# Kernel tuning notes

Measured on AMD Instinct MI355X. Metric: run time of the kernel, lower is better.

Reference implementation:

```python
import jax, jax.numpy as jnp
import numpy as np
from jax import lax

PROB_THRESHOLD = 0.9
IOU_THRESHOLD = 0.5
H, W = 80, 80


def setup_inputs() -> dict:
    key = jax.random.key(0)
    # [5, H, W]: channel 0 = probability, channels 1:5 = (x1, y1, w, h)
    x = jax.random.uniform(key, (5, H, W), dtype=jnp.float32)
    return {"x": x}


def _pairwise_iou(boxes):
    # boxes: [N, 4] in xyxy format (torchvision box_iou semantics, no +1)
    area = jnp.maximum(boxes[:, 2] - boxes[:, 0], 0.0) * jnp.maximum(boxes[:, 3] - boxes[:, 1], 0.0)
    lt = jnp.maximum(boxes[:, None, :2], boxes[None, :, :2])  # [N, N, 2]
    rb = jnp.minimum(boxes[:, None, 2:], boxes[None, :, 2:])  # [N, N, 2]
    wh = jnp.maximum(rb - lt, 0.0)
    inter = wh[..., 0] * wh[..., 1]                           # [N, N]
    union = area[:, None] + area[None, :] - inter
    return inter / jnp.maximum(union, 1e-9)


def reference(x):
    # Flatten grid: rows = [prob, x1, y1, w, h]
    flat = x.reshape(5, -1).T  # [N, 5]
    valid = flat[:, 0] > PROB_THRESHOLD

    # Faithful in-place transform from the torch code:
    #   bbx[:, 2] = bbx[:, 0] + bbx[:, 2];  bbx[:, 3] = bbx[:, 1] + bbx[:, 3]
    # (column 0 is the probability channel, exactly as the source does it)
    c2 = flat[:, 0] + flat[:, 2]
    c3 = flat[:, 1] + flat[:, 3]
    b5 = jnp.stack([flat[:, 0], flat[:, 1], c2, c3, flat[:, 4]], axis=1)  # [N, 5]

    # Sort by score descending; invalid rows pushed to the end with -inf
    scores = jnp.where(valid, b5[:, 0], -jnp.inf)
    order = jnp.argsort(-scores)
    b5_sorted = b5[order]          # [N, 5]
    valid_sorted = valid[order]    # [N]
    boxes = b5_sorted[:, 1:]       # [N, 4] -> nms(boxes=x[:,1:], scores=x[:,0])

    iou = _pairwise_iou(boxes)     # [N, N], dominant 164 MB intermediate
    N = boxes.shape[0]

    # Greedy NMS in score order: keep box i iff it is valid and no already-kept
    # higher-scoring box overlaps it with IoU > threshold.
    def body(i, keep):
        suppressed = jnp.any(keep & (iou[i] > IOU_THRESHOLD))
        return keep.at[i].set(valid_sorted[i] & ~suppressed)

    keep = lax.fori_loop(0, N, body, jnp.zeros((N,), dtype=bool))

    # Fixed-shape, jit-friendly equivalent of x[bbxis]: kept rows (score-sorted),
    # suppressed / below-threshold rows zeroed out.
    return jnp.where(keep[:, None], b5_sorted, 0.0)
```

## Files before the change

### kernel.cpp

```cpp
#include <hip/hip_runtime.h>


#define MAXM  256
#define CHUNK 200

__global__ __launch_bounds__(256) void k_rankpart(
    const float* __restrict__ X, int* __restrict__ part,
    int* __restrict__ counters, int n, int groups, int chunks) {
  int b = blockIdx.x;
  if (b >= groups * chunks) {
    if (threadIdx.x < 8) counters[threadIdx.x] = 0;
    return;
  }
  int g = b / chunks, c = b - g * chunks;
  int i = g * 256 + threadIdx.x;
  int c0 = c * CHUNK, cend = min(c0 + CHUNK, n);
  float si = (i < n) ? X[i] : -1.f;
  int gt = 0, eq = 0;
  const float4* X4 = (const float4*)(X + c0);
  int nq = (cend - c0) >> 2;
  for (int q = 0; q < nq; ++q) {
    float4 v = X4[q];
    gt += (v.x > si) + (v.y > si) + (v.z > si) + (v.w > si);
    eq += (v.x == si) + (v.y == si) + (v.z == si) + (v.w == si);
  }
  for (int j = c0 + (nq << 2); j < cend; ++j) {
    float sj = X[j];
    gt += (sj > si); eq += (sj == si);
  }
  if (i >= c0 && i < cend) eq -= 1;
  int partial = gt;
  if (__any(eq > 0)) {
    int eqlt = 0;
    for (int j = c0; j < cend; ++j)
      eqlt += (X[j] == si) && (j < i);
    partial = gt + eqlt;
  }
  if (i < n) part[c * n + i] = partial;
}

__global__ __launch_bounds__(256) void k_finish(
    const float* __restrict__ X, const int* __restrict__ part,
    float* __restrict__ out, float* __restrict__ list,
    int* __restrict__ counters, int n, int chunks, int nblocks) {
  __shared__ int sfix;
  const int t = threadIdx.x;
  int i = blockIdx.x * 256 + t;
  if (i < n) {
    float s = X[i];
    int r = 0;
    for (int c = 0; c < chunks; ++c) r += part[c * n + i];
    float* row = out + (size_t)r * 5;
    if (s > 0.9f) {
      float f1 = X[n + i], f2 = X[2 * n + i], f3 = X[3 * n + i], f4 = X[4 * n + i];
      float c2 = s + f2, c3 = f1 + f3;
      row[0] = s; row[1] = f1; row[2] = c2; row[3] = c3; row[4] = f4;
      float w = fmaxf(c3 - f1, 0.f);
      float h = fmaxf(f4 - c2, 0.f);
      float area = w * h;
      if (area > 0.f) {
        int p = atomicAdd(&counters[0], 1);
        if (p < MAXM) {
          float* e = list + (size_t)p * 6;
          e[0] = __int_as_float(r);
          e[1] = f1; e[2] = c2; e[3] = c3; e[4] = f4; e[5] = area;
        }
      }
    } else {
      row[0] = 0.f; row[1] = 0.f; row[2] = 0.f; row[3] = 0.f; row[4] = 0.f;
    }
  }
  __threadfence();
  __syncthreads();
  if (t == 0) {
    int old = atomicAdd(&counters[1], 1);
    sfix = (old == nblocks - 1);
  }
  __syncthreads();
  if (!sfix) return;
  __threadfence();

  __shared__ int   srank[MAXM];
  __shared__ float sbox[MAXM][4];
  __shared__ float sarea[MAXM];
  __shared__ int   skeep[MAXM];
  __shared__ int   sflag;
  int M = __hip_atomic_load(&counters[0], __ATOMIC_ACQUIRE, __HIP_MEMORY_SCOPE_AGENT);
  if (M > MAXM) M = MAXM;
  for (int e = t; e < M; e += 256) {
    float v0 = __hip_atomic_load(&list[e * 6 + 0], __ATOMIC_RELAXED, __HIP_MEMORY_SCOPE_AGENT);
    int r = __float_as_int(v0);
    int pos = 0;
    for (int m = 0; m < M; ++m) {
      float vm = __hip_atomic_load(&list[m * 6 + 0], __ATOMIC_RELAXED, __HIP_MEMORY_SCOPE_AGENT);
      pos += (__float_as_int(vm) < r);
    }
    srank[pos] = r;
    sbox[pos][0] = __hip_atomic_load(&list[e * 6 + 1], __ATOMIC_RELAXED, __HIP_MEMORY_SCOPE_AGENT);
    sbox[pos][1] = __hip_atomic_load(&list[e * 6 + 2], __ATOMIC_RELAXED, __HIP_MEMORY_SCOPE_AGENT);
    sbox[pos][2] = __hip_atomic_load(&list[e * 6 + 3], __ATOMIC_RELAXED, __HIP_MEMORY_SCOPE_AGENT);
    sbox[pos][3] = __hip_atomic_load(&list[e * 6 + 4], __ATOMIC_RELAXED, __HIP_MEMORY_SCOPE_AGENT);
    sarea[pos]   = __hip_atomic_load(&list[e * 6 + 5], __ATOMIC_RELAXED, __HIP_MEMORY_SCOPE_AGENT);
    skeep[pos] = 1;
  }
  __syncthreads();
  for (int s = 1; s < M; ++s) {
    if (t == 0) sflag = 0;
    __syncthreads();
    if (t < s && skeep[t]) {
      float ltx = fmaxf(sbox[t][0], sbox[s][0]);
      float lty = fmaxf(sbox[t][1], sbox[s][1]);
      float rbx = fminf(sbox[t][2], sbox[s][2]);
      float rby = fminf(sbox[t][3], sbox[s][3]);
      float w = fmaxf(rbx - ltx, 0.f);
      float h = fmaxf(rby - lty, 0.f);
      float inter = w * h;
      float uni = sarea[t] + sarea[s] - inter;
      if (inter / fmaxf(uni, 1e-9f) > 0.5f) sflag = 1;
    }
    __syncthreads();
    if (t == 0 && sflag) skeep[s] = 0;
    __syncthreads();
  }
  for (int e = t; e < M; e += 256) {
    if (!skeep[e]) {
      float* row = out + (size_t)srank[e] * 5;
      row[0] = 0.f; row[1] = 0.f; row[2] = 0.f; row[3] = 0.f; row[4] = 0.f;
    }
  }
}

#define FB_NTH  1024
#define FB_MAXV 2048
__global__ __launch_bounds__(FB_NTH, 1) void nms_fallback(
    const float* __restrict__ X, float* __restrict__ out, int n, int out_n) {
  __shared__ float cscore[FB_MAXV];
  __shared__ unsigned int cidx[FB_MAXV];
  __shared__ int s_vcount, s_mcount, sflag;
  __shared__ int srank[MAXM];
  __shared__ float sbox[MAXM][4];
  __shared__ float sarea[MAXM];
  __shared__ int skeep[MAXM];
  __shared__ int prank[MAXM];
  __shared__ float pbox[MAXM][4];
  __shared__ float parea[MAXM];
  const int t = threadIdx.x;
  if (t == 0) { s_vcount = 0; s_mcount = 0; }
  float4* out4 = (float4*)out;
  int n4 = out_n >> 2;
  for (int i = t; i < n4; i += FB_NTH) out4[i] = make_float4(0.f, 0.f, 0.f, 0.f);
  for (int i = (n4 << 2) + t; i < out_n; i += FB_NTH) out[i] = 0.f;
  __syncthreads();
  for (int i = t; i < n; i += FB_NTH) {
    float s = X[i];
    if (s > 0.9f) {
      int p = atomicAdd(&s_vcount, 1);
      if (p < FB_MAXV) { cscore[p] = s; cidx[p] = (unsigned int)i; }
    }
  }
  __syncthreads();
  const int V = min(s_vcount, FB_MAXV);
  for (int e = t; e < V; e += FB_NTH) {
    float s = cscore[e];
    unsigned int idx = cidx[e];
    int rank = 0;
    for (int m = 0; m < V; ++m) {
      float sm = cscore[m];
      rank += (sm > s) || (sm == s && cidx[m] < idx);
    }
    float f1 = X[n + idx], f2 = X[2 * n + idx], f3 = X[3 * n + idx], f4 = X[4 * n + idx];
    float c2 = s + f2, c3 = f1 + f3;
    float* row = out + (size_t)rank * 5;
    row[0] = s; row[1] = f1; row[2] = c2; row[3] = c3; row[4] = f4;
    float w = fmaxf(c3 - f1, 0.f), h = fmaxf(f4 - c2, 0.f);
    float area = w * h;
    if (area > 0.f) {
      int p = atomicAdd(&s_mcount, 1);
      if (p < MAXM) {
        prank[p] = rank;
        pbox[p][0] = f1; pbox[p][1] = c2; pbox[p][2] = c3; pbox[p][3] = f4;
        parea[p] = area;
      }
    }
  }
  __syncthreads();
  const int M = min(s_mcount, MAXM);
  for (int e = t; e < M; e += FB_NTH) {
    int r = prank[e];
    int pos = 0;
    for (int m = 0; m < M; ++m) pos += (prank[m] < r);
    srank[pos] = r;
    sbox[pos][0] = pbox[e][0]; sbox[pos][1] = pbox[e][1];
    sbox[pos][2] = pbox[e][2]; sbox[pos][3] = pbox[e][3];
    sarea[pos] = parea[e];
    skeep[pos] = 1;
  }
  __syncthreads();
  for (int s = 1; s < M; ++s) {
    if (t == 0) sflag = 0;
    __syncthreads();
    if (t < s && skeep[t]) {
      float ltx = fmaxf(sbox[t][0], sbox[s][0]);
      float lty = fmaxf(sbox[t][1], sbox[s][1]);
      float rbx = fminf(sbox[t][2], sbox[s][2]);
      float rby = fminf(sbox[t][3], sbox[s][3]);
      float w = fmaxf(rbx - ltx, 0.f), h = fmaxf(rby - lty, 0.f);
      float inter = w * h;
      float uni = sarea[t] + sarea[s] - inter;
      if (inter / fmaxf(uni, 1e-9f) > 0.5f) sflag = 1;
    }
    __syncthreads();
    if (t == 0 && sflag) skeep[s] = 0;
    __syncthreads();
  }
  for (int e = t; e < M; e += FB_NTH) {
    if (!skeep[e]) {
      float* row = out + (size_t)srank[e] * 5;
      row[0] = 0.f; row[1] = 0.f; row[2] = 0.f; row[3] = 0.f; row[4] = 0.f;
    }
  }
}

extern "C" void kernel_launch(void* const* d_in, const int* in_sizes, int n_in,
                              void* d_out, int out_size, void* d_ws, size_t ws_size,
                              hipStream_t stream) {
  const float* X = (const float*)d_in[0];
  float* out = (float*)d_out;
  int n = in_sizes[0] / 5;
  int groups = (n + 255) / 256;
  int chunks = (n + CHUNK - 1) / CHUNK;
  size_t part_bytes = (size_t)chunks * n * sizeof(int);
  size_t need = 256 + part_bytes + (size_t)MAXM * 6 * sizeof(float);
  if (ws_size >= need) {
    int* counters = (int*)d_ws;
    int* part = (int*)((char*)d_ws + 256);
    float* list = (float*)((char*)d_ws + 256 + part_bytes);
    hipLaunchKernelGGL(k_rankpart, dim3(groups * chunks + 1), dim3(256), 0, stream,
                       X, part, counters, n, groups, chunks);
    hipLaunchKernelGGL(k_finish, dim3(groups), dim3(256), 0, stream,
                       X, part, out, list, counters, n, chunks, groups);
  } else {
    hipLaunchKernelGGL(nms_fallback, dim3(1), dim3(FB_NTH), 0, stream, X, out, n, out_size);
  }
}
```

Before: 79.31 us.

## Rank only valid boxes via shared-memory key compaction in each block

Replaces the all-pairs partial rank pass and the separate finish kernel with one kernel. Every block compacts the above-threshold scores into shared memory as packed 64-bit (score, ~index) keys, then ranks only its own share of valid boxes against that list. Rows past the valid count are zero-filled in parallel, and a single-block fix kernel runs greedy NMS over the candidate boxes indexed by rank. This removes the O(n^2) rank work and the partial-rank buffer, at the cost of every block re-scanning the score channel and the fix kernel scanning a flag array of length V.

Result: faster. 73.77 us (-7.0%).

```diff
diff --git a/kernel.cpp b/kernel.cpp
--- a/kernel.cpp
+++ b/kernel.cpp
@@ -1,130 +1,141 @@
 #include <hip/hip_runtime.h>
 
 
-#define MAXM  256
-#define CHUNK 200
-
-__global__ __launch_bounds__(256) void k_rankpart(
-    const float* __restrict__ X, int* __restrict__ part,
-    int* __restrict__ counters, int n, int groups, int chunks) {
-  int b = blockIdx.x;
-  if (b >= groups * chunks) {
-    if (threadIdx.x < 8) counters[threadIdx.x] = 0;
-    return;
-  }
-  int g = b / chunks, c = b - g * chunks;
-  int i = g * 256 + threadIdx.x;
-  int c0 = c * CHUNK, cend = min(c0 + CHUNK, n);
-  float si = (i < n) ? X[i] : -1.f;
-  int gt = 0, eq = 0;
-  const float4* X4 = (const float4*)(X + c0);
-  int nq = (cend - c0) >> 2;
-  for (int q = 0; q < nq; ++q) {
+#define MAXM   1024
+#define MAXW   512
+#define MAXKEY 6400
+
+__global__ __launch_bounds__(256) void k_main(
+    const float* __restrict__ X, float* __restrict__ out,
+    int* __restrict__ vout, int* __restrict__ flags, float* __restrict__ list,
+    int n, int out_n) {
+  __shared__ unsigned long long skey[MAXKEY];
+  __shared__ int swork[MAXW];
+  __shared__ int lcnt, wcnt;
+  const int t = threadIdx.x, b = blockIdx.x, nb = gridDim.x;
+  if (t == 0) { lcnt = 0; wcnt = 0; }
+  __syncthreads();
+
+  const float4* X4 = (const float4*)X;
+  int nq = n >> 2;
+  for (int q = t; q < nq; q += 256) {
     float4 v = X4[q];
-    gt += (v.x > si) + (v.y > si) + (v.z > si) + (v.w > si);
-    eq += (v.x == si) + (v.y == si) + (v.z == si) + (v.w == si);
-  }
-  for (int j = c0 + (nq << 2); j < cend; ++j) {
-    float sj = X[j];
-    gt += (sj > si); eq += (sj == si);
-  }
-  if (i >= c0 && i < cend) eq -= 1;
-  int partial = gt;
-  if (__any(eq > 0)) {
-    int eqlt = 0;
-    for (int j = c0; j < cend; ++j)
-      eqlt += (X[j] == si) && (j < i);
-    partial = gt + eqlt;
-  }
-  if (i < n) part[c * n + i] = partial;
-}
-
-__global__ __launch_bounds__(256) void k_finish(
-    const float* __restrict__ X, const int* __restrict__ part,
-    float* __restrict__ out, float* __restrict__ list,
-    int* __restrict__ counters, int n, int chunks, int nblocks) {
-  __shared__ int sfix;
-  const int t = threadIdx.x;
-  int i = blockIdx.x * 256 + t;
-  if (i < n) {
-    float s = X[i];
-    int r = 0;
-    for (int c = 0; c < chunks; ++c) r += part[c * n + i];
-    float* row = out + (size_t)r * 5;
-    if (s > 0.9f) {
-      float f1 = X[n + i], f2 = X[2 * n + i], f3 = X[3 * n + i], f4 = X[4 * n + i];
-      float c2 = s + f2, c3 = f1 + f3;
-      row[0] = s; row[1] = f1; row[2] = c2; row[3] = c3; row[4] = f4;
-      float w = fmaxf(c3 - f1, 0.f);
-      float h = fmaxf(f4 - c2, 0.f);
-      float area = w * h;
-      if (area > 0.f) {
-        int p = atomicAdd(&counters[0], 1);
-        if (p < MAXM) {
-          float* e = list + (size_t)p * 6;
-          e[0] = __int_as_float(r);
-          e[1] = f1; e[2] = c2; e[3] = c3; e[4] = f4; e[5] = area;
+    int i0 = q << 2;
+    float vs[4] = {v.x, v.y, v.z, v.w};
+#pragma unroll
+    for (int c = 0; c < 4; ++c) {
+      if (vs[c] > 0.9f) {
+        int i = i0 + c;
+        int p = atomicAdd(&lcnt, 1);
+        if (p < MAXKEY)
+          skey[p] = ((unsigned long long)__float_as_uint(vs[c]) << 32) |
+                    (unsigned int)(~i);
+        if ((i % nb) == b) {
+          int w = atomicAdd(&wcnt, 1);
+          if (w < MAXW) swork[w] = i;
         }
       }
+    }
+  }
+  for (int i = (nq << 2) + t; i < n; i += 256) {
+    float s = X[i];
+    if (s > 0.9f) {
+      int p = atomicAdd(&lcnt, 1);
+      if (p < MAXKEY)
+        skey[p] = ((unsigned long long)__float_as_uint(s) << 32) |
+                  (unsigned int)(~i);
+      if ((i % nb) == b) {
+        int w = atomicAdd(&wcnt, 1);
+        if (w < MAXW) swork[w] = i;
+      }
+    }
+  }
+  __syncthreads();
+  const int V = min(lcnt, MAXKEY);
+  if (b == 0 && t == 0) *vout = V;
+
+  const int W = min(wcnt, MAXW);
+  for (int e = t; e < W; e += 256) {
+    int i = swork[e];
+    float s  = X[i];
+    float f1 = X[n + i], f2 = X[2 * n + i], f3 = X[3 * n + i], f4 = X[4 * n + i];
+    unsigned long long Ke =
+        ((unsigned long long)__float_as_uint(s) << 32) | (unsigned int)(~i);
+    int rank = 0;
+    for (int m = 0; m < V; ++m)
+      rank += (skey[m] > Ke);
+    float c2 = s + f2, c3 = f1 + f3;
+    float w = fmaxf(c3 - f1, 0.f);
+    float h = fmaxf(f4 - c2, 0.f);
+    float area = w * h;
+    if (area > 0.f) {
+      float* L = list + (size_t)rank * 8;
+      L[0] = s; L[1] = f1; L[2] = c2; L[3] = c3; L[4] = f4; L[5] = area;
+      flags[rank] = 1;
     } else {
-      row[0] = 0.f; row[1] = 0.f; row[2] = 0.f; row[3] = 0.f; row[4] = 0.f;
-    }
-  }
-  __threadfence();
-  __syncthreads();
-  if (t == 0) {
-    int old = atomicAdd(&counters[1], 1);
-    sfix = (old == nblocks - 1);
-  }
-  __syncthreads();
-  if (!sfix) return;
-  __threadfence();
-
-  __shared__ int   srank[MAXM];
-  __shared__ float sbox[MAXM][4];
-  __shared__ float sarea[MAXM];
+      float* row = out + (size_t)rank * 5;
+      row[0] = s; row[1] = f1; row[2] = c2; row[3] = c3; row[4] = f4;
+      flags[rank] = 0;
+    }
+  }
+
+  for (int f = 5 * V + b * 256 + t; f < out_n; f += nb * 256)
+    out[f] = 0.f;
+}
+
+__global__ __launch_bounds__(256) void k_fix(
+    const float* __restrict__ list, const int* __restrict__ flags,
+    const int* __restrict__ vptr, float* __restrict__ out) {
+  __shared__ int   sm, sflag;
+  __shared__ int   sr[MAXM];
+  __shared__ int   sord[MAXM];
+  __shared__ float sb[MAXM][5];
+  __shared__ float sa[MAXM];
   __shared__ int   skeep[MAXM];
-  __shared__ int   sflag;
-  int M = __hip_atomic_load(&counters[0], __ATOMIC_ACQUIRE, __HIP_MEMORY_SCOPE_AGENT);
-  if (M > MAXM) M = MAXM;
+  const int t = threadIdx.x;
+  if (t == 0) sm = 0;
+  __syncthreads();
+  const int V = *vptr;
+  for (int r = t; r < V; r += 256)
+    if (flags[r]) { int p = atomicAdd(&sm, 1); if (p < MAXM) sr[p] = r; }
+  __syncthreads();
+  const int M = min(sm, MAXM);
   for (int e = t; e < M; e += 256) {
-    float v0 = __hip_atomic_load(&list[e * 6 + 0], __ATOMIC_RELAXED, __HIP_MEMORY_SCOPE_AGENT);
-    int r = __float_as_int(v0);
+    int r = sr[e];
     int pos = 0;
-    for (int m = 0; m < M; ++m) {
-      float vm = __hip_atomic_load(&list[m * 6 + 0], __ATOMIC_RELAXED, __HIP_MEMORY_SCOPE_AGENT);
-      pos += (__float_as_int(vm) < r);
-    }
-    srank[pos] = r;
-    sbox[pos][0] = __hip_atomic_load(&list[e * 6 + 1], __ATOMIC_RELAXED, __HIP_MEMORY_SCOPE_AGENT);
-    sbox[pos][1] = __hip_atomic_load(&list[e * 6 + 2], __ATOMIC_RELAXED, __HIP_MEMORY_SCOPE_AGENT);
-    sbox[pos][2] = __hip_atomic_load(&list[e * 6 + 3], __ATOMIC_RELAXED, __HIP_MEMORY_SCOPE_AGENT);
-    sbox[pos][3] = __hip_atomic_load(&list[e * 6 + 4], __ATOMIC_RELAXED, __HIP_MEMORY_SCOPE_AGENT);
-    sarea[pos]   = __hip_atomic_load(&list[e * 6 + 5], __ATOMIC_RELAXED, __HIP_MEMORY_SCOPE_AGENT);
+    for (int m = 0; m < M; ++m) pos += (sr[m] < r);
+    const float* L = list + (size_t)r * 8;
+    sord[pos] = r;
+    sb[pos][0] = L[0]; sb[pos][1] = L[1]; sb[pos][2] = L[2];
+    sb[pos][3] = L[3]; sb[pos][4] = L[4];
+    sa[pos] = L[5];
     skeep[pos] = 1;
   }
   __syncthreads();
-  for (int s = 1; s < M; ++s) {
+  for (int i = 1; i < M; ++i) {
     if (t == 0) sflag = 0;
     __syncthreads();
-    if (t < s && skeep[t]) {
-      float ltx = fmaxf(sbox[t][0], sbox[s][0]);
-      float lty = fmaxf(sbox[t][1], sbox[s][1]);
-      float rbx = fminf(sbox[t][2], sbox[s][2]);
-      float rby = fminf(sbox[t][3], sbox[s][3]);
+    if (t < i && skeep[t]) {
+      float ltx = fmaxf(sb[t][1], sb[i][1]);
+      float lty = fmaxf(sb[t][2], sb[i][2]);
+      float rbx = fminf(sb[t][3], sb[i][3]);
+      float rby = fminf(sb[t][4], sb[i][4]);
       float w = fmaxf(rbx - ltx, 0.f);
       float h = fmaxf(rby - lty, 0.f);
       float inter = w * h;
-      float uni = sarea[t] + sarea[s] - inter;
+      float uni = sa[t] + sa[i] - inter;
       if (inter / fmaxf(uni, 1e-9f) > 0.5f) sflag = 1;
     }
     __syncthreads();
-    if (t == 0 && sflag) skeep[s] = 0;
+    if (t == 0 && sflag) skeep[i] = 0;
     __syncthreads();
   }
   for (int e = t; e < M; e += 256) {
-    if (!skeep[e]) {
-      float* row = out + (size_t)srank[e] * 5;
+    float* row = out + (size_t)sord[e] * 5;
+    if (skeep[e]) {
+      row[0] = sb[e][0]; row[1] = sb[e][1]; row[2] = sb[e][2];
+      row[3] = sb[e][3]; row[4] = sb[e][4];
+    } else {
       row[0] = 0.f; row[1] = 0.f; row[2] = 0.f; row[3] = 0.f; row[4] = 0.f;
     }
   }
@@ -132,18 +143,19 @@
 
 #define FB_NTH  1024
 #define FB_MAXV 2048
+#define FB_MAXM 256
 __global__ __launch_bounds__(FB_NTH, 1) void nms_fallback(
     const float* __restrict__ X, float* __restrict__ out, int n, int out_n) {
   __shared__ float cscore[FB_MAXV];
   __shared__ unsigned int cidx[FB_MAXV];
   __shared__ int s_vcount, s_mcount, sflag;
-  __shared__ int srank[MAXM];
-  __shared__ float sbox[MAXM][4];
-  __shared__ float sarea[MAXM];
-  __shared__ int skeep[MAXM];
-  __shared__ int prank[MAXM];
-  __shared__ float pbox[MAXM][4];
-  __shared__ float parea[MAXM];
+  __shared__ int srank[FB_MAXM];
+  __shared__ float sbox[FB_MAXM][4];
+  __shared__ float sarea[FB_MAXM];
+  __shared__ int skeep[FB_MAXM];
+  __shared__ int prank[FB_MAXM];
+  __shared__ float pbox[FB_MAXM][4];
+  __shared__ float parea[FB_MAXM];
   const int t = threadIdx.x;
   if (t == 0) { s_vcount = 0; s_mcount = 0; }
   float4* out4 = (float4*)out;
@@ -176,7 +188,7 @@
     float area = w * h;
     if (area > 0.f) {
       int p = atomicAdd(&s_mcount, 1);
-      if (p < MAXM) {
+      if (p < FB_MAXM) {
         prank[p] = rank;
         pbox[p][0] = f1; pbox[p][1] = c2; pbox[p][2] = c3; pbox[p][3] = f4;
         parea[p] = area;
@@ -184,7 +196,7 @@
     }
   }
   __syncthreads();
-  const int M = min(s_mcount, MAXM);
+  const int M = min(s_mcount, FB_MAXM);
   for (int e = t; e < M; e += FB_NTH) {
     int r = prank[e];
     int pos = 0;
@@ -227,18 +239,18 @@
   const float* X = (const float*)d_in[0];
   float* out = (float*)d_out;
   int n = in_sizes[0] / 5;
-  int groups = (n + 255) / 256;
-  int chunks = (n + CHUNK - 1) / CHUNK;
-  size_t part_bytes = (size_t)chunks * n * sizeof(int);
-  size_t need = 256 + part_bytes + (size_t)MAXM * 6 * sizeof(float);
-  if (ws_size >= need) {
-    int* counters = (int*)d_ws;
-    int* part = (int*)((char*)d_ws + 256);
-    float* list = (float*)((char*)d_ws + 256 + part_bytes);
-    hipLaunchKernelGGL(k_rankpart, dim3(groups * chunks + 1), dim3(256), 0, stream,
-                       X, part, counters, n, groups, chunks);
-    hipLaunchKernelGGL(k_finish, dim3(groups), dim3(256), 0, stream,
-                       X, part, out, list, counters, n, chunks, groups);
+  int nb = (n + 255) / 256;
+  size_t flags_off = 256;
+  size_t list_off = (flags_off + (size_t)n * sizeof(int) + 15) & ~(size_t)15;
+  size_t need = list_off + (size_t)n * 8 * sizeof(float);
+  if (ws_size >= need && n <= MAXKEY) {
+    int* vout = (int*)d_ws;
+    int* flags = (int*)((char*)d_ws + flags_off);
+    float* list = (float*)((char*)d_ws + list_off);
+    hipLaunchKernelGGL(k_main, dim3(nb), dim3(256), 0, stream,
+                       X, out, vout, flags, list, n, out_size);
+    hipLaunchKernelGGL(k_fix, dim3(1), dim3(256), 0, stream,
+                       list, flags, vout, out);
   } else {
     hipLaunchKernelGGL(nms_fallback, dim3(1), dim3(FB_NTH), 0, stream, X, out, n, out_size);
   }
```

## Replace last-block atomic handoff with a dedicated NMS block in finish kernel

Applied to the files above, without the earlier changes.

The finish kernel no longer uses a global atomic list, threadfences and a last-block-done counter to pick the block that runs NMS. Instead, one extra block scans the scores itself, collects candidate boxes with positive area, rebuilds their ranks from the partial-rank buffer, and runs the greedy suppression while the other blocks scatter the rows that need no NMS. The rank kernel switches to a 2D grid with larger chunks, and the counter-reset block is removed. The aim is to drop cross-block synchronisation and the serial tail. The cost is duplicated candidate filtering in one block, and the suppression loop still assumes at most 256 candidates even though MAXM is now 1024.

Result: slower. 90.02 us (+13.5%).

```diff
diff --git a/kernel.cpp b/kernel.cpp
--- a/kernel.cpp
+++ b/kernel.cpp
@@ -1,24 +1,18 @@
 #include <hip/hip_runtime.h>
 
 
-#define MAXM  256
-#define CHUNK 200
+#define CHUNK 400
+#define MAXM  1024
 
 __global__ __launch_bounds__(256) void k_rankpart(
-    const float* __restrict__ X, int* __restrict__ part,
-    int* __restrict__ counters, int n, int groups, int chunks) {
-  int b = blockIdx.x;
-  if (b >= groups * chunks) {
-    if (threadIdx.x < 8) counters[threadIdx.x] = 0;
-    return;
-  }
-  int g = b / chunks, c = b - g * chunks;
-  int i = g * 256 + threadIdx.x;
-  int c0 = c * CHUNK, cend = min(c0 + CHUNK, n);
+    const float* __restrict__ X, int* __restrict__ part, int n, int chunks) {
+  const int c = blockIdx.x, g = blockIdx.y;
+  const int i = g * 256 + threadIdx.x;
+  const int c0 = c * CHUNK, cend = min(c0 + CHUNK, n);
   float si = (i < n) ? X[i] : -1.f;
   int gt = 0, eq = 0;
   const float4* X4 = (const float4*)(X + c0);
-  int nq = (cend - c0) >> 2;
+  const int nq = (cend - c0) >> 2;
   for (int q = 0; q < nq; ++q) {
     float4 v = X4[q];
     gt += (v.x > si) + (v.y > si) + (v.z > si) + (v.w > si);
@@ -41,90 +35,98 @@
 
 __global__ __launch_bounds__(256) void k_finish(
     const float* __restrict__ X, const int* __restrict__ part,
-    float* __restrict__ out, float* __restrict__ list,
-    int* __restrict__ counters, int n, int chunks, int nblocks) {
-  __shared__ int sfix;
-  const int t = threadIdx.x;
-  int i = blockIdx.x * 256 + t;
-  if (i < n) {
-    float s = X[i];
+    float* __restrict__ out, int n, int chunks, int groups) {
+  const int t = threadIdx.x, b = blockIdx.x;
+
+  if (b < groups) {
+    int i = b * 256 + t;
+    if (i >= n) return;
     int r = 0;
     for (int c = 0; c < chunks; ++c) r += part[c * n + i];
+    float s = X[i];
     float* row = out + (size_t)r * 5;
     if (s > 0.9f) {
       float f1 = X[n + i], f2 = X[2 * n + i], f3 = X[3 * n + i], f4 = X[4 * n + i];
       float c2 = s + f2, c3 = f1 + f3;
-      row[0] = s; row[1] = f1; row[2] = c2; row[3] = c3; row[4] = f4;
       float w = fmaxf(c3 - f1, 0.f);
       float h = fmaxf(f4 - c2, 0.f);
-      float area = w * h;
-      if (area > 0.f) {
-        int p = atomicAdd(&counters[0], 1);
-        if (p < MAXM) {
-          float* e = list + (size_t)p * 6;
-          e[0] = __int_as_float(r);
-          e[1] = f1; e[2] = c2; e[3] = c3; e[4] = f4; e[5] = area;
-        }
-      }
+      if (w * h > 0.f) return;
+      row[0] = s; row[1] = f1; row[2] = c2; row[3] = c3; row[4] = f4;
     } else {
       row[0] = 0.f; row[1] = 0.f; row[2] = 0.f; row[3] = 0.f; row[4] = 0.f;
     }
-  }
-  __threadfence();
-  __syncthreads();
-  if (t == 0) {
-    int old = atomicAdd(&counters[1], 1);
-    sfix = (old == nblocks - 1);
-  }
-  __syncthreads();
-  if (!sfix) return;
-  __threadfence();
-
-  __shared__ int   srank[MAXM];
-  __shared__ float sbox[MAXM][4];
-  __shared__ float sarea[MAXM];
-  __shared__ int   skeep[MAXM];
-  __shared__ int   sflag;
-  int M = __hip_atomic_load(&counters[0], __ATOMIC_ACQUIRE, __HIP_MEMORY_SCOPE_AGENT);
-  if (M > MAXM) M = MAXM;
+    return;
+  }
+
+  __shared__ int   mcnt, sflag;
+  __shared__ int   cand[MAXM];
+  __shared__ int   srnk[MAXM];
+  __shared__ int   ornk[MAXM];
+  __shared__ float obox[MAXM][5];
+  __shared__ float oarea[MAXM];
+  __shared__ int   okeep[MAXM];
+  if (t == 0) mcnt = 0;
+  __syncthreads();
+  for (int i = t; i < n; i += 256) {
+    float s = X[i];
+    if (s > 0.9f) {
+      float f1 = X[n + i], f2 = X[2 * n + i], f3 = X[3 * n + i], f4 = X[4 * n + i];
+      float c2 = s + f2, c3 = f1 + f3;
+      float w = fmaxf(c3 - f1, 0.f);
+      float h = fmaxf(f4 - c2, 0.f);
+      if (w * h > 0.f) {
+        int p = atomicAdd(&mcnt, 1);
+        if (p < MAXM) cand[p] = i;
+      }
+    }
+  }
+  __syncthreads();
+  const int M = min(mcnt, MAXM);
+  if (M == 0) return;
   for (int e = t; e < M; e += 256) {
-    float v0 = __hip_atomic_load(&list[e * 6 + 0], __ATOMIC_RELAXED, __HIP_MEMORY_SCOPE_AGENT);
-    int r = __float_as_int(v0);
+    int i = cand[e];
+    int r = 0;
+    for (int c = 0; c < chunks; ++c) r += part[c * n + i];
+    srnk[e] = r;
+  }
+  __syncthreads();
+  for (int e = t; e < M; e += 256) {
+    int r = srnk[e], i = cand[e];
     int pos = 0;
-    for (int m = 0; m < M; ++m) {
-      float vm = __hip_atomic_load(&list[m * 6 + 0], __ATOMIC_RELAXED, __HIP_MEMORY_SCOPE_AGENT);
-      pos += (__float_as_int(vm) < r);
-    }
-    srank[pos] = r;
-    sbox[pos][0] = __hip_atomic_load(&list[e * 6 + 1], __ATOMIC_RELAXED, __HIP_MEMORY_SCOPE_AGENT);
-    sbox[pos][1] = __hip_atomic_load(&list[e * 6 + 2], __ATOMIC_RELAXED, __HIP_MEMORY_SCOPE_AGENT);
-    sbox[pos][2] = __hip_atomic_load(&list[e * 6 + 3], __ATOMIC_RELAXED, __HIP_MEMORY_SCOPE_AGENT);
-    sbox[pos][3] = __hip_atomic_load(&list[e * 6 + 4], __ATOMIC_RELAXED, __HIP_MEMORY_SCOPE_AGENT);
-    sarea[pos]   = __hip_atomic_load(&list[e * 6 + 5], __ATOMIC_RELAXED, __HIP_MEMORY_SCOPE_AGENT);
-    skeep[pos] = 1;
-  }
-  __syncthreads();
-  for (int s = 1; s < M; ++s) {
+    for (int m = 0; m < M; ++m) pos += (srnk[m] < r);
+    float s = X[i], f1 = X[n + i], f2 = X[2 * n + i], f3 = X[3 * n + i], f4 = X[4 * n + i];
+    float c2 = s + f2, c3 = f1 + f3;
+    ornk[pos] = r;
+    obox[pos][0] = s; obox[pos][1] = f1; obox[pos][2] = c2;
+    obox[pos][3] = c3; obox[pos][4] = f4;
+    oarea[pos] = fmaxf(c3 - f1, 0.f) * fmaxf(f4 - c2, 0.f);
+    okeep[pos] = 1;
+  }
+  __syncthreads();
+  for (int i = 1; i < M; ++i) {
     if (t == 0) sflag = 0;
     __syncthreads();
-    if (t < s && skeep[t]) {
-      float ltx = fmaxf(sbox[t][0], sbox[s][0]);
-      float lty = fmaxf(sbox[t][1], sbox[s][1]);
-      float rbx = fminf(sbox[t][2], sbox[s][2]);
-      float rby = fminf(sbox[t][3], sbox[s][3]);
+    if (t < i && okeep[t]) {
+      float ltx = fmaxf(obox[t][1], obox[i][1]);
+      float lty = fmaxf(obox[t][2], obox[i][2]);
+      float rbx = fminf(obox[t][3], obox[i][3]);
+      float rby = fminf(obox[t][4], obox[i][4]);
       float w = fmaxf(rbx - ltx, 0.f);
       float h = fmaxf(rby - lty, 0.f);
       float inter = w * h;
-      float uni = sarea[t] + sarea[s] - inter;
+      float uni = oarea[t] + oarea[i] - inter;
       if (inter / fmaxf(uni, 1e-9f) > 0.5f) sflag = 1;
     }
     __syncthreads();
-    if (t == 0 && sflag) skeep[s] = 0;
+    if (t == 0 && sflag) okeep[i] = 0;
     __syncthreads();
   }
   for (int e = t; e < M; e += 256) {
-    if (!skeep[e]) {
-      float* row = out + (size_t)srank[e] * 5;
+    float* row = out + (size_t)ornk[e] * 5;
+    if (okeep[e]) {
+      row[0] = obox[e][0]; row[1] = obox[e][1]; row[2] = obox[e][2];
+      row[3] = obox[e][3]; row[4] = obox[e][4];
+    } else {
       row[0] = 0.f; row[1] = 0.f; row[2] = 0.f; row[3] = 0.f; row[4] = 0.f;
     }
   }
@@ -132,18 +134,19 @@
 
 #define FB_NTH  1024
 #define FB_MAXV 2048
+#define FB_MAXM 256
 __global__ __launch_bounds__(FB_NTH, 1) void nms_fallback(
     const float* __restrict__ X, float* __restrict__ out, int n, int out_n) {
   __shared__ float cscore[FB_MAXV];
   __shared__ unsigned int cidx[FB_MAXV];
   __shared__ int s_vcount, s_mcount, sflag;
-  __shared__ int srank[MAXM];
-  __shared__ float sbox[MAXM][4];
-  __shared__ float sarea[MAXM];
-  __shared__ int skeep[MAXM];
-  __shared__ int prank[MAXM];
-  __shared__ float pbox[MAXM][4];
-  __shared__ float parea[MAXM];
+  __shared__ int srank[FB_MAXM];
+  __shared__ float sbox[FB_MAXM][4];
+  __shared__ float sarea[FB_MAXM];
+  __shared__ int skeep[FB_MAXM];
+  __shared__ int prank[FB_MAXM];
+  __shared__ float pbox[FB_MAXM][4];
+  __shared__ float parea[FB_MAXM];
   const int t = threadIdx.x;
   if (t == 0) { s_vcount = 0; s_mcount = 0; }
   float4* out4 = (float4*)out;
@@ -176,7 +179,7 @@
     float area = w * h;
     if (area > 0.f) {
       int p = atomicAdd(&s_mcount, 1);
-      if (p < MAXM) {
+      if (p < FB_MAXM) {
         prank[p] = rank;
         pbox[p][0] = f1; pbox[p][1] = c2; pbox[p][2] = c3; pbox[p][3] = f4;
         parea[p] = area;
@@ -184,7 +187,7 @@
     }
   }
   __syncthreads();
-  const int M = min(s_mcount, MAXM);
+  const int M = min(s_mcount, FB_MAXM);
   for (int e = t; e < M; e += FB_NTH) {
     int r = prank[e];
     int pos = 0;
@@ -229,16 +232,13 @@
   int n = in_sizes[0] / 5;
   int groups = (n + 255) / 256;
   int chunks = (n + CHUNK - 1) / CHUNK;
-  size_t part_bytes = (size_t)chunks * n * sizeof(int);
-  size_t need = 256 + part_bytes + (size_t)MAXM * 6 * sizeof(float);
+  size_t need = (size_t)chunks * n * sizeof(int);
   if (ws_size >= need) {
-    int* counters = (int*)d_ws;
-    int* part = (int*)((char*)d_ws + 256);
-    float* list = (float*)((char*)d_ws + 256 + part_bytes);
-    hipLaunchKernelGGL(k_rankpart, dim3(groups * chunks + 1), dim3(256), 0, stream,
-                       X, part, counters, n, groups, chunks);
-    hipLaunchKernelGGL(k_finish, dim3(groups), dim3(256), 0, stream,
-                       X, part, out, list, counters, n, chunks, groups);
+    int* part = (int*)d_ws;
+    hipLaunchKernelGGL(k_rankpart, dim3(chunks, groups), dim3(256), 0, stream,
+                       X, part, n, chunks);
+    hipLaunchKernelGGL(k_finish, dim3(groups + 1), dim3(256), 0, stream,
+                       X, part, out, n, chunks, groups);
   } else {
     hipLaunchKernelGGL(nms_fallback, dim3(1), dim3(FB_NTH), 0, stream, X, out, n, out_size);
   }
```
